# Kernel tuning notes

Hardware: AMD Instinct MI355X
Metric: run time of the kernel (lower is better)

The kernel has to match this reference:

```python
import jax, jax.numpy as jnp
import numpy as np

B, T, NHANDS, DKP = 8, 1024, 2, 128
DM, H, DH, DFF, V, M, L = 1024, 16, 64, 4096, 2000, 256, 2
KEPS = 1e-4  # performer feature-map epsilon


def _orth_proj(key, m, d):
    # Gaussian orthogonal random features (FAVOR+), rows rescaled to chi norms
    n_blocks = int(np.ceil(m / d))
    blocks = []
    for i in range(n_blocks):
        q, _ = jnp.linalg.qr(jax.random.normal(jax.random.fold_in(key, i), (d, d)))
        blocks.append(q.T)
    mat = jnp.concatenate(blocks, 0)[:m]
    mult = jnp.linalg.norm(jax.random.normal(jax.random.fold_in(key, 10 ** 6), (m, d)), axis=1)
    return (mat * mult[:, None]).astype(jnp.float32)


def setup_inputs() -> dict:
    key = jax.random.key(0)
    ks = iter(jax.random.split(key, 64))
    w = lambda shape, s=0.02: (jax.random.normal(next(ks), shape) * s).astype(jnp.float32)
    z = lambda *shape: jnp.zeros(shape, jnp.float32)
    o = lambda *shape: jnp.ones(shape, jnp.float32)
    return {
        'x': jax.random.normal(next(ks), (B, T, NHANDS, DKP), dtype=jnp.float32),
        'Win': w((NHANDS * DKP, DM)), 'b_in': z(DM),
        'pe': jax.random.normal(next(ks), (5000, DM), dtype=jnp.float32),
        'ln1_g': o(L, DM), 'ln1_b': z(L, DM),
        'Wq': w((L, DM, DM)), 'bq': z(L, DM),
        'Wk': w((L, DM, DM)), 'bk': z(L, DM),
        'Wv': w((L, DM, DM)), 'bv': z(L, DM),
        'Wo': w((L, DM, DM)), 'bo': z(L, DM),
        'ln2_g': o(L, DM), 'ln2_b': z(L, DM),
        'W1': w((L, DM, DFF)), 'b1': z(L, DFF),
        'W2': w((L, DFF, DM)), 'b2': z(L, DM),
        'Wc': w((DM, V)), 'bc': z(V),
        'Wconv': w((64, DM, 3)), 'bconv': z(64),
        'Waux': w((64, V + 1)), 'baux': z(V + 1),
        'proj': _orth_proj(next(ks), M, DH),
    }


def _ln(x, g, b):
    mu = jnp.mean(x, -1, keepdims=True)
    var = jnp.mean((x - mu) ** 2, -1, keepdims=True)
    return (x - mu) / jnp.sqrt(var + 1e-5) * g + b


def _feats(data, proj, is_query):
    # FAVOR+ softmax kernel features, data: (B,H,T,DH) -> (B,H,T,M)
    dn = DH ** -0.25
    ratio = M ** -0.5
    dd = jnp.einsum('bhnd,md->bhnm', data, proj) * dn
    diag = jnp.sum(data ** 2, -1, keepdims=True) * 0.5 * dn * dn
    if is_query:
        stab = jnp.max(dd, -1, keepdims=True)
    else:
        stab = jnp.max(dd, (-1, -2), keepdims=True)
    return ratio * (jnp.exp(dd - diag - jax.lax.stop_gradient(stab)) + KEPS)


def reference(x, Win, b_in, pe, ln1_g, ln1_b, Wq, bq, Wk, bk, Wv, bv, Wo, bo,
              ln2_g, ln2_b, W1, b1, W2, b2, Wc, bc, Wconv, bconv, Waux, baux, proj):
    h = x.reshape(B, T, NHANDS * DKP) @ Win + b_in
    h = h + pe[:T][None]

    def layer(h, i):
        y = _ln(h, ln1_g[i], ln1_b[i])
        q = (y @ Wq[i] + bq[i]).reshape(B, T, H, DH).transpose(0, 2, 1, 3)
        k = (y @ Wk[i] + bk[i]).reshape(B, T, H, DH).transpose(0, 2, 1, 3)
        v = (y @ Wv[i] + bv[i]).reshape(B, T, H, DH).transpose(0, 2, 1, 3)
        qp = _feats(q, proj, True)   # (B,H,T,M)
        kp = _feats(k, proj, False)
        dinv = 1.0 / jnp.einsum('bhnm,bhm->bhn', qp, kp.sum(2))
        ctx = jnp.einsum('bhnm,bhnd->bhmd', kp, v)          # (B,H,M,DH)
        o = jnp.einsum('bhnm,bhmd->bhnd', qp, ctx) * dinv[..., None]
        o = o.transpose(0, 2, 1, 3).reshape(B, T, DM) @ Wo[i] + bo[i]
        h = h + o
        y = _ln(h, ln2_g[i], ln2_b[i])
        ff = jax.nn.gelu(y @ W1[i] + b1[i], approximate=False) @ W2[i] + b2[i]
        return h + ff

    h = layer(h, 0)
    xa = h.transpose(0, 2, 1)  # (B, DM, T)
    xa = jax.lax.conv_general_dilated(xa, Wconv, (1,), 'SAME',
                                      dimension_numbers=('NCH', 'OIH', 'NCH'))
    xa = xa + bconv[None, :, None]
    aux = xa.transpose(0, 2, 1) @ Waux + baux  # (B, T, V+1)
    h = layer(h, 1)
    gloss = h @ Wc + bc  # (B, T, V)
    return (gloss, aux)
```

## Files before the change

kernel.cpp:

```cpp
#include <hip/hip_runtime.h>
#include <hip/hip_bf16.h>

typedef __attribute__((ext_vector_type(4))) float f32x4;
typedef __attribute__((ext_vector_type(8))) unsigned short u16x8;
typedef __attribute__((ext_vector_type(4))) unsigned short u16x4;
typedef __bf16 bf16x8 __attribute__((ext_vector_type(8)));

#define DEVFN static __device__ __forceinline__

constexpr int CB = 8, CT = 1024, CDM = 1024, CH = 16, CDH = 64, CDFF = 4096, CV = 2000, CM = 256;
constexpr int CNT = CB * CT;
constexpr int CQKV = 3072;
constexpr float CDN = 0.35355339059327373f;
constexpr float CRATIO = 0.0625f;
constexpr float CKEPS = 1e-4f;

DEVFN unsigned short f2bu(float x) {
  __hip_bfloat16 h = __float2bfloat16(x);
  return __builtin_bit_cast(unsigned short, h);
}
DEVFN float b2f(unsigned short u) {
  __hip_bfloat16 h = __builtin_bit_cast(__hip_bfloat16, u);
  return __bfloat162float(h);
}
DEVFN float wredsum(float s) {
#pragma unroll
  for (int ofs = 32; ofs; ofs >>= 1) s += __shfl_xor(s, ofs, 64);
  return s;
}
DEVFN float wredmax(float s) {
#pragma unroll
  for (int ofs = 32; ofs; ofs >>= 1) s = fmaxf(s, __shfl_xor(s, ofs, 64));
  return s;
}
DEVFN void gl_lds16(const void* g, void* l) {
  __builtin_amdgcn_global_load_lds(
      (const __attribute__((address_space(1))) unsigned int*)g,
      (__attribute__((address_space(3))) unsigned int*)l, 16, 0, 0);
}
DEVFN f32x4 mfma16(u16x8 a, u16x8 b, f32x4 c) {
  return __builtin_amdgcn_mfma_f32_16x16x32_bf16(
      __builtin_bit_cast(bf16x8, a), __builtin_bit_cast(bf16x8, b), c, 0, 0, 0);
}
DEVFN u16x8 lds_rd128(unsigned addr) {
  u16x8 r;
  asm volatile("ds_read_b128 %0, %1" : "=v"(r) : "v"(addr));
  return r;
}
DEVFN unsigned lds_addr(const void* p) {
  return (unsigned)(unsigned long)(const __attribute__((address_space(3))) char*)p;
}

#define EPI_BIAS 1
#define EPI_ACCUM 2
#define EPI_GELU 4
#define EPI_OUTBF 8
#define EPI_PE 32
#define EPI_DUP 64

template <int EPI>
__global__ __launch_bounds__(512, 6) void gemm32_k(
    const unsigned short* __restrict__ A, const unsigned short* __restrict__ Bt,
    const float* __restrict__ bias, void* __restrict__ C, void* __restrict__ aux,
    int Mr, int Nr, int Kr, int lda, int ldb, int ldc) {
  __shared__ unsigned short smA[2][128 * 32];
  __shared__ unsigned short smB[2][128 * 32];

  int tid = threadIdx.x, wv = tid >> 6, ll = tid & 63;
  int wm = wv >> 2, wn = wv & 3;
  int m0 = blockIdx.x * 128, n0 = blockIdx.y * 128;
  int fr = ll & 15, f16 = ll >> 4, fk = f16 * 8;

  const char* Ab = (const char*)A;
  const char* Bb = (const char*)Bt;

  unsigned int offA, offB;
  {
    int L = tid * 16;
    int P = L ^ (((L >> 9) & 1) << 5);
    int r = P >> 6, cb = P & 63;
    long rowA = min(m0 + r, Mr - 1);
    offA = (unsigned)(rowA * lda * 2 + cb);
    long rowB = min(n0 + r, Nr - 1);
    offB = (unsigned)(rowB * ldb * 2 + cb);
  }
  unsigned aAb = lds_addr(&smA[0][0]), aBb = lds_addr(&smB[0][0]);
  unsigned offArd[4], offBrd[2];
#pragma unroll
  for (int i = 0; i < 4; i++) {
    int r = wm * 64 + i * 16 + fr;
    offArd[i] = aAb + (unsigned)(r * 64 + 2 * (fk ^ (((r >> 3) & 1) << 4)));
  }
#pragma unroll
  for (int j = 0; j < 2; j++) {
    int r = wn * 32 + j * 16 + fr;
    offBrd[j] = aBb + (unsigned)(r * 64 + 2 * (fk ^ (((r >> 3) & 1) << 4)));
  }

  f32x4 acc[4][2] = {};
  int NT = Kr / 32;

#define STG32(PB, KBN)                                                       \
  {                                                                          \
    gl_lds16(Ab + offA + (KBN), &smA[PB][tid * 8]);                          \
    gl_lds16(Bb + offB + (KBN), &smB[PB][tid * 8]);                          \
  }
#define TILE32(PB, KBN)                                                      \
  {                                                                          \
    __builtin_amdgcn_s_barrier();              \
    __builtin_amdgcn_sched_barrier(0);                                       \
    STG32((PB) ^ 1, KBN);                                                    \
    asm volatile("s_waitcnt vmcnt(2)" ::: "memory");                         \
    __builtin_amdgcn_sched_barrier(0);                                       \
    __builtin_amdgcn_s_barrier();                 \
    __builtin_amdgcn_sched_barrier(0);                                       \
    u16x8 a[4], b0, b1;                                                      \
    _Pragma("unroll") for (int i = 0; i < 4; i++)                            \
        a[i] = lds_rd128(offArd[i] + (PB)*8192);                             \
    b0 = lds_rd128(offBrd[0] + (PB)*8192);                                   \
    b1 = lds_rd128(offBrd[1] + (PB)*8192);                                   \
    asm volatile("s_waitcnt lgkmcnt(1)" ::: "memory");                       \
    __builtin_amdgcn_sched_barrier(0);                                       \
    __builtin_amdgcn_s_setprio(1);                                           \
    _Pragma("unroll") for (int i = 0; i < 4; i++)                            \
        acc[i][0] = mfma16(a[i], b0, acc[i][0]);                             \
    __builtin_amdgcn_s_setprio(0);                                           \
    asm volatile("s_waitcnt lgkmcnt(0)" ::: "memory");                       \
    __builtin_amdgcn_sched_barrier(0);                                       \
    __builtin_amdgcn_s_setprio(1);                                           \
    _Pragma("unroll") for (int i = 0; i < 4; i++)                            \
        acc[i][1] = mfma16(a[i], b1, acc[i][1]);                             \
    __builtin_amdgcn_s_setprio(0);                                           \
  }

  STG32(0, 0);
  for (int t = 0; t < NT; t += 2) {
    long kb1 = (long)(t + 1) * 64;
    long kb2 = (long)min(t + 2, NT - 1) * 64;
    TILE32(0, kb1);
    TILE32(1, kb2);
  }
  asm volatile("s_waitcnt vmcnt(0)" ::: "memory");
  __builtin_amdgcn_sched_barrier(0);
#undef TILE32
#undef STG32

#pragma unroll
  for (int i = 0; i < 4; i++) {
#pragma unroll
    for (int j = 0; j < 2; j++) {
#pragma unroll
      for (int e = 0; e < 4; e++) {
        int gr = m0 + wm * 64 + i * 16 + f16 * 4 + e;
        int gc = n0 + wn * 32 + j * 16 + fr;
        if (gr < Mr && gc < Nr) {
          float v = acc[i][j][e];
          if (EPI & EPI_BIAS) v += bias[gc];
          if (EPI & EPI_GELU) v = 0.5f * v * (1.0f + erff(v * 0.70710678118f));
          if (EPI & EPI_PE) v += ((const float*)aux)[((long)(gr & 1023) << 10) + gc];
          long idx = (long)gr * ldc + gc;
          if (EPI & EPI_ACCUM) v += ((float*)C)[idx];
          if (EPI & EPI_OUTBF) ((unsigned short*)C)[idx] = f2bu(v);
          else ((float*)C)[idx] = v;
          if (EPI & EPI_DUP) ((unsigned short*)aux)[idx] = f2bu(v);
        }
      }
    }
  }
}

template <int EPI>
__global__ __launch_bounds__(512, 4) void gemm128_k(
    const unsigned short* __restrict__ A, const unsigned short* __restrict__ Bt,
    const float* __restrict__ bias, void* __restrict__ C, void* __restrict__ aux,
    int Mr, int Nr, int Kr, int lda, int ldb, int ldc) {
  __shared__ unsigned short smA[2][128 * 64];
  __shared__ unsigned short smB[2][128 * 64];

  int tid = threadIdx.x, wv = tid >> 6, ll = tid & 63;
  int wm = wv >> 2, wn = wv & 3;
  int m0 = blockIdx.x * 128, n0 = blockIdx.y * 128;
  int fr = ll & 15, f16 = ll >> 4, fk = f16 * 8;

  const char* Ab = (const char*)A;
  const char* Bb = (const char*)Bt;

  unsigned int offA[2], offB[2];
#pragma unroll
  for (int ro = 0; ro < 2; ro++) {
    int L = (ro * 512 + tid) * 16;
    int P = L ^ (((L >> 9) & 1) << 5);
    int kh = P >> 13, rem = P & 8191;
    int r = rem >> 6, cb = rem & 63;
    long rowA = min(m0 + r, Mr - 1);
    offA[ro] = (unsigned)((rowA * lda + kh * 32) * 2 + cb);
    long rowB = min(n0 + r, Nr - 1);
    offB[ro] = (unsigned)((rowB * ldb + kh * 32) * 2 + cb);
  }
  unsigned aAb = lds_addr(&smA[0][0]), aBb = lds_addr(&smB[0][0]);
  unsigned offArd[4], offBrd[2];
#pragma unroll
  for (int i = 0; i < 4; i++) {
    int r = wm * 64 + i * 16 + fr;
    offArd[i] = aAb + (unsigned)(r * 64 + 2 * (fk ^ (((r >> 3) & 1) << 4)));
  }
#pragma unroll
  for (int j = 0; j < 2; j++) {
    int r = wn * 32 + j * 16 + fr;
    offBrd[j] = aBb + (unsigned)(r * 64 + 2 * (fk ^ (((r >> 3) & 1) << 4)));
  }

  f32x4 acc[4][2] = {};
  int NT = Kr / 64;

#define STGALL(PB, KBN)                                                      \
  {                                                                          \
    _Pragma("unroll") for (int ro = 0; ro < 2; ro++)                         \
        gl_lds16(Ab + offA[ro] + (KBN), &smA[PB][(ro * 512 + wv * 64) * 8]); \
    _Pragma("unroll") for (int ro = 0; ro < 2; ro++)                         \
        gl_lds16(Bb + offB[ro] + (KBN), &smB[PB][(ro * 512 + wv * 64) * 8]); \
  }
#define TILE(PB, KBN)                                                        \
  {                                                                          \
    __builtin_amdgcn_s_barrier();                                            \
    __builtin_amdgcn_sched_barrier(0);                                       \
    STGALL((PB) ^ 1, KBN);                                                   \
    asm volatile("s_waitcnt vmcnt(4)" ::: "memory");                         \
    __builtin_amdgcn_sched_barrier(0);                                       \
    __builtin_amdgcn_s_barrier();                                            \
    __builtin_amdgcn_sched_barrier(0);                                       \
    u16x8 a0[4], b0[2], a1[4], b1[2];                                        \
    _Pragma("unroll") for (int i = 0; i < 4; i++)                            \
        a0[i] = lds_rd128(offArd[i] + (PB)*16384);                           \
    _Pragma("unroll") for (int j = 0; j < 2; j++)                            \
        b0[j] = lds_rd128(offBrd[j] + (PB)*16384);                           \
    _Pragma("unroll") for (int i = 0; i < 4; i++)                            \
        a1[i] = lds_rd128(offArd[i] + (PB)*16384 + 8192);                    \
    _Pragma("unroll") for (int j = 0; j < 2; j++)                            \
        b1[j] = lds_rd128(offBrd[j] + (PB)*16384 + 8192);                    \
    asm volatile("s_waitcnt lgkmcnt(6)" ::: "memory");                       \
    __builtin_amdgcn_sched_barrier(0);                                       \
    __builtin_amdgcn_s_setprio(1);                                           \
    _Pragma("unroll") for (int i = 0; i < 4; i++) {                          \
      acc[i][0] = mfma16(a0[i], b0[0], acc[i][0]);                           \
      acc[i][1] = mfma16(a0[i], b0[1], acc[i][1]);                           \
    }                                                                        \
    __builtin_amdgcn_s_setprio(0);                                           \
    asm volatile("s_waitcnt lgkmcnt(0)" ::: "memory");                       \
    __builtin_amdgcn_sched_barrier(0);                                       \
    __builtin_amdgcn_s_setprio(1);                                           \
    _Pragma("unroll") for (int i = 0; i < 4; i++) {                          \
      acc[i][0] = mfma16(a1[i], b1[0], acc[i][0]);                           \
      acc[i][1] = mfma16(a1[i], b1[1], acc[i][1]);                           \
    }                                                                        \
    __builtin_amdgcn_s_setprio(0);                                           \
  }

  STGALL(0, 0);
  for (int t = 0; t < NT; t += 2) {
    long kb1 = (long)(t + 1) * 128;
    long kb2 = (long)min(t + 2, NT - 1) * 128;
    TILE(0, kb1);
    TILE(1, kb2);
  }
  asm volatile("s_waitcnt vmcnt(0)" ::: "memory");
  __builtin_amdgcn_sched_barrier(0);
#undef TILE
#undef STGALL

#pragma unroll
  for (int i = 0; i < 4; i++) {
#pragma unroll
    for (int j = 0; j < 2; j++) {
#pragma unroll
      for (int e = 0; e < 4; e++) {
        int gr = m0 + wm * 64 + i * 16 + f16 * 4 + e;
        int gc = n0 + wn * 32 + j * 16 + fr;
        if (gr < Mr && gc < Nr) {
          float v = acc[i][j][e];
          if (EPI & EPI_BIAS) v += bias[gc];
          if (EPI & EPI_GELU) v = 0.5f * v * (1.0f + erff(v * 0.70710678118f));
          if (EPI & EPI_PE) v += ((const float*)aux)[((long)(gr & 1023) << 10) + gc];
          long idx = (long)gr * ldc + gc;
          if (EPI & EPI_ACCUM) v += ((float*)C)[idx];
          if (EPI & EPI_OUTBF) ((unsigned short*)C)[idx] = f2bu(v);
          else ((float*)C)[idx] = v;
          if (EPI & EPI_DUP) ((unsigned short*)aux)[idx] = f2bu(v);
        }
      }
    }
  }
}

template <int EPI, int MB, int NB>
__global__ __launch_bounds__(256) void gemm_k(
    const unsigned short* __restrict__ Aall, const unsigned short* __restrict__ Btall,
    const float* __restrict__ bias, void* __restrict__ Call,
    int Mr, int Nr, int Kr, int lda, int ldb, int ldc, int bdiv,
    long As1, long As2, long Bs1, long Bs2, long Cs1, long Cs2) {
  __shared__ unsigned short smA[MB * 32];
  __shared__ unsigned short smB[NB * 32];
  constexpr int WRN = (MB == 128 && NB == 128) ? 2 : (MB == 128 ? 4 : 1);
  constexpr int WCN = 4 / WRN;
  constexpr int MT = MB / WRN, NTW = NB / WCN;
  constexpr int AF = MT / 16, BF = NTW / 16;
  int bz = blockIdx.z;
  const unsigned short* A = Aall + (long)(bz / bdiv) * As1 + (long)(bz % bdiv) * As2;
  const unsigned short* Bt = Btall + (long)(bz / bdiv) * Bs1 + (long)(bz % bdiv) * Bs2;
  long coff = (long)(bz / bdiv) * Cs1 + (long)(bz % bdiv) * Cs2;

  int tid = threadIdx.x, wv = tid >> 6, ll = tid & 63;
  int m0 = blockIdx.x * MB, n0 = blockIdx.y * NB;
  int sr = tid >> 2, sc = (tid & 3) * 8;
  long ar0 = min(m0 + sr, Mr - 1);
  long ar1 = (MB == 128) ? min(m0 + sr + 64, (long)Mr - 1) : 0;
  long br0 = min(n0 + sr, Nr - 1);
  long br1 = (NB == 128) ? min(n0 + sr + 64, (long)Nr - 1) : 0;
  unsigned short* lA0 = &smA[(wv * 16) * 32];
  unsigned short* lA1 = &smA[(64 + wv * 16) * 32];
  unsigned short* lB0 = &smB[(wv * 16) * 32];
  unsigned short* lB1 = &smB[(64 + wv * 16) * 32];

  f32x4 acc[AF][BF] = {};
  int wr = (WRN == 1) ? 0 : ((WRN == 2) ? (wv >> 1) * MT : wv * MT);
  int wc = (WCN == 1) ? 0 : ((WCN == 2) ? (wv & 1) * NTW : wv * NTW);
  int fr = ll & 15, fk = (ll >> 4) * 8;

  for (int k0 = 0; k0 < Kr; k0 += 32) {
    __syncthreads();
    gl_lds16(A + ar0 * lda + k0 + sc, lA0);
    if (MB == 128) gl_lds16(A + ar1 * lda + k0 + sc, lA1);
    gl_lds16(Bt + br0 * ldb + k0 + sc, lB0);
    if (NB == 128) gl_lds16(Bt + br1 * ldb + k0 + sc, lB1);
    __syncthreads();
    u16x8 af[AF], bfr[BF];
#pragma unroll
    for (int i = 0; i < AF; i++) af[i] = *(const u16x8*)&smA[(wr + i * 16 + fr) * 32 + fk];
#pragma unroll
    for (int j = 0; j < BF; j++) bfr[j] = *(const u16x8*)&smB[(wc + j * 16 + fr) * 32 + fk];
#pragma unroll
    for (int i = 0; i < AF; i++)
#pragma unroll
      for (int j = 0; j < BF; j++) acc[i][j] = mfma16(af[i], bfr[j], acc[i][j]);
  }

#pragma unroll
  for (int i = 0; i < AF; i++) {
#pragma unroll
    for (int j = 0; j < BF; j++) {
#pragma unroll
      for (int e = 0; e < 4; e++) {
        int gr = m0 + wr + i * 16 + (ll >> 4) * 4 + e;
        int gc = n0 + wc + j * 16 + (ll & 15);
        if (gr < Mr && gc < Nr) {
          float v = acc[i][j][e];
          if (EPI & EPI_BIAS) v += bias[gc];
          long idx = coff + (long)gr * ldc + gc;
          if (EPI & EPI_OUTBF) ((unsigned short*)Call)[idx] = f2bu(v);
          else ((float*)Call)[idx] = v;
        }
      }
    }
  }
}

DEVFN void feat_dd(const unsigned short* __restrict__ src, const unsigned short* __restrict__ projc,
                   unsigned short* ldsq, unsigned short* ldsp, int b, int t0, int hh,
                   f32x4 acc[16]) {
  int tid = threadIdx.x, wv = tid >> 6, ll = tid & 63;
#pragma unroll
  for (int p = 0; p < 2; p++) {
    int r = p * 64 + (tid >> 3), c8 = (tid & 7) * 8;
    *(u16x8*)&ldsq[r * 72 + c8] =
        *(const u16x8*)&src[((long)b * CT + t0 + r) * CQKV + hh * CDH + c8];
  }
#pragma unroll
  for (int p = 0; p < 4; p++) {
    int r = p * 64 + (tid >> 3), c8 = (tid & 7) * 8;
    *(u16x8*)&ldsp[r * 72 + c8] = *(const u16x8*)&projc[r * 64 + c8];
  }
  __syncthreads();
  int fr = ll & 15, fk = (ll >> 4) * 8;
#pragma unroll
  for (int ks = 0; ks < 2; ks++) {
    u16x8 af = *(const u16x8*)&ldsq[(wv * 16 + fr) * 72 + ks * 32 + fk];
#pragma unroll
    for (int j = 0; j < 16; j++) {
      u16x8 bf = *(const u16x8*)&ldsp[(j * 16 + fr) * 72 + ks * 32 + fk];
      acc[j] = mfma16(af, bf, acc[j]);
    }
  }
}

__global__ __launch_bounds__(512, 4) void kstab_f(const unsigned short* __restrict__ kb,
                                                  const unsigned short* __restrict__ projc,
                                                  const unsigned short* __restrict__ vb,
                                                  float* __restrict__ part,
                                                  unsigned short* __restrict__ vt) {
  extern __shared__ char dynsm[];
  unsigned short* ldsq = (unsigned short*)dynsm;
  unsigned short* ldsp = (unsigned short*)(dynsm + 18432);
  __shared__ float smx[8];
  int tid = threadIdx.x;
  int bh = blockIdx.x >> 3, chunk = blockIdx.x & 7;
  int b = bh >> 4, hh = bh & 15;
  int t0 = chunk * 128;
  f32x4 acc[16] = {};
  feat_dd(kb, projc, ldsq, ldsp, b, t0, hh, acc);
  float mx = -3.4e38f;
#pragma unroll
  for (int j = 0; j < 16; j++)
#pragma unroll
    for (int e = 0; e < 4; e++) mx = fmaxf(mx, acc[j][e]);
  mx = wredmax(mx);
  int wv = tid >> 6;
  if ((tid & 63) == 0) smx[wv] = mx;
  __syncthreads();
  if (tid == 0) {
    float m2 = smx[0];
#pragma unroll
    for (int i = 1; i < 8; i++) m2 = fmaxf(m2, smx[i]);
    part[blockIdx.x] = m2;
  }
#pragma unroll
  for (int p = 0; p < 2; p++) {
    int r = p * 64 + (tid >> 3), c8 = (tid & 7) * 8;
    *(u16x8*)&ldsq[r * 72 + c8] =
        *(const u16x8*)&vb[((long)b * CT + t0 + r) * CQKV + hh * CDH + c8];
  }
  __syncthreads();
  int d = tid >> 3, tz = (tid & 7) * 16;
  unsigned short o1[8], o2[8];
#pragma unroll
  for (int e = 0; e < 8; e++) {
    o1[e] = ldsq[(tz + e) * 72 + d];
    o2[e] = ldsq[(tz + 8 + e) * 72 + d];
  }
  long vbase = ((long)bh * CDH + d) * CT + t0 + tz;
  *(u16x8*)&vt[vbase] = *(u16x8*)&o1[0];
  *(u16x8*)&vt[vbase + 8] = *(u16x8*)&o2[0];
}

__global__ __launch_bounds__(512, 4) void featk_f(const unsigned short* __restrict__ kb,
                                                  const unsigned short* __restrict__ projc,
                                                  const float* __restrict__ part,
                                                  unsigned short* __restrict__ kpt,
                                                  float* __restrict__ kspart) {
  extern __shared__ char dynsm[];
  unsigned short* ldsq = (unsigned short*)dynsm;
  unsigned short* ldsp = (unsigned short*)(dynsm + 18432);
  unsigned short* ldso = (unsigned short*)dynsm;
  int tid = threadIdx.x, wv = tid >> 6, ll = tid & 63;
  int bh = blockIdx.x >> 3, chunk = blockIdx.x & 7;
  int b = bh >> 4, hh = bh & 15;
  float st = part[bh * 8];
#pragma unroll
  for (int i = 1; i < 8; i++) st = fmaxf(st, part[bh * 8 + i]);
  f32x4 acc[16] = {};
  feat_dd(kb, projc, ldsq, ldsp, b, chunk * 128, hh, acc);
  int fr = ll & 15, g = ll >> 4;
  float diag[4];
#pragma unroll
  for (int e = 0; e < 4; e++) {
    int row = wv * 16 + g * 4 + e;
    u16x4 kv = *(const u16x4*)&ldsq[row * 72 + fr * 4];
    float s = 0;
#pragma unroll
    for (int z = 0; z < 4; z++) { float f = b2f(kv[z]); s += f * f; }
#pragma unroll
    for (int o = 1; o < 16; o <<= 1) s += __shfl_xor(s, o, 64);
    diag[e] = s * (0.5f * CDN * CDN);
  }
  __syncthreads();
#pragma unroll
  for (int j = 0; j < 16; j++)
#pragma unroll
    for (int e = 0; e < 4; e++) {
      float v = CRATIO * (expf(acc[j][e] - diag[e] - st) + CKEPS);
      ldso[(j * 16 + fr) * 136 + wv * 16 + g * 4 + e] = f2bu(v);
    }
  __syncthreads();
  int m = tid >> 1, seg = (tid & 1) * 64;
  long base = ((long)bh * CM + m) * CT + chunk * 128;
  float ks = 0;
#pragma unroll
  for (int z = 0; z < 8; z++) {
    u16x8 v8 = *(u16x8*)&ldso[m * 136 + seg + z * 8];
    *(u16x8*)&kpt[base + seg + z * 8] = v8;
#pragma unroll
    for (int w = 0; w < 8; w++) ks += b2f(v8[w]);
  }
  ks += __shfl_xor(ks, 1, 64);
  if ((tid & 1) == 0) kspart[((long)bh * 8 + chunk) * CM + m] = ks;
}

__global__ __launch_bounds__(512, 4) void featqo_f(const unsigned short* __restrict__ qb,
                                                   const unsigned short* __restrict__ projc,
                                                   const float* __restrict__ kspart,
                                                   const unsigned short* __restrict__ ctxall,
                                                   unsigned short* __restrict__ obuf) {
  extern __shared__ char dynsm[];
  unsigned short* ldsq = (unsigned short*)dynsm;
  unsigned short* ldsp = (unsigned short*)(dynsm + 18432);
  unsigned short* ldso = (unsigned short*)dynsm;
  float* ldks = (float*)(dynsm + 67584);
  float* ldinv = (float*)(dynsm + 68608);
  int tid = threadIdx.x, wv = tid >> 6, ll = tid & 63;
  int bh = blockIdx.x >> 3, chunk = blockIdx.x & 7;
  int b = bh >> 4, hh = bh & 15;
  int t0 = chunk * 128;
  if (tid < 256) {
    float s = 0;
#pragma unroll
    for (int c = 0; c < 8; c++) s += kspart[((long)bh * 8 + c) * CM + tid];
    ldks[tid] = s;
  }
  f32x4 acc[16] = {};
  feat_dd(qb, projc, ldsq, ldsp, b, t0, hh, acc);
  int fr = ll & 15, g = ll >> 4, fk = g * 8;
  float rmax[4], diag[4];
#pragma unroll
  for (int e = 0; e < 4; e++) {
    float mx = acc[0][e];
#pragma unroll
    for (int j = 1; j < 16; j++) mx = fmaxf(mx, acc[j][e]);
#pragma unroll
    for (int o = 1; o < 16; o <<= 1) mx = fmaxf(mx, __shfl_xor(mx, o, 64));
    rmax[e] = mx;
    int row = wv * 16 + g * 4 + e;
    u16x4 qv = *(const u16x4*)&ldsq[row * 72 + fr * 4];
    float s = 0;
#pragma unroll
    for (int z = 0; z < 4; z++) { float f = b2f(qv[z]); s += f * f; }
#pragma unroll
    for (int o = 1; o < 16; o <<= 1) s += __shfl_xor(s, o, 64);
    diag[e] = s * (0.5f * CDN * CDN);
  }
  __syncthreads();
#pragma unroll
  for (int j = 0; j < 16; j++)
#pragma unroll
    for (int e = 0; e < 4; e++) {
      float v = CRATIO * (expf(acc[j][e] - diag[e] - rmax[e]) + CKEPS);
      ldso[(wv * 16 + g * 4 + e) * 264 + j * 16 + fr] = f2bu(v);
    }
  __syncthreads();
  {
    int row = tid >> 2, seg = (tid & 3) * 64;
    float dot = 0;
#pragma unroll
    for (int z = 0; z < 8; z++) {
      u16x8 v8 = *(u16x8*)&ldso[row * 264 + seg + z * 8];
#pragma unroll
      for (int w = 0; w < 8; w++) dot += b2f(v8[w]) * ldks[seg + z * 8 + w];
    }
    dot += __shfl_xor(dot, 1, 64);
    dot += __shfl_xor(dot, 2, 64);
    if ((tid & 3) == 0) ldinv[row] = 1.0f / dot;
  }
  const unsigned short* ctxb = ctxall + (long)bh * 16384;
  f32x4 ao[4] = {};
#pragma unroll
  for (int ks = 0; ks < 8; ks++) {
    u16x8 af = *(const u16x8*)&ldso[(wv * 16 + fr) * 264 + ks * 32 + fk];
#pragma unroll
    for (int j = 0; j < 4; j++) {
      u16x8 bf = *(const u16x8*)&ctxb[(j * 16 + fr) * 256 + ks * 32 + fk];
      ao[j] = mfma16(af, bf, ao[j]);
    }
  }
  __syncthreads();
#pragma unroll
  for (int j = 0; j < 4; j++)
#pragma unroll
    for (int e = 0; e < 4; e++) {
      int r = wv * 16 + g * 4 + e;
      float v = ao[j][e] * ldinv[r];
      obuf[((long)b * CT + t0 + r) * CDM + hh * CDH + j * 16 + fr] = f2bu(v);
    }
}

__global__ __launch_bounds__(256) void ln_k(const float* __restrict__ h,
                                            const float* __restrict__ g,
                                            const float* __restrict__ b,
                                            unsigned short* __restrict__ y) {
  int wv = threadIdx.x >> 6, ll = threadIdx.x & 63;
  long row = (long)blockIdx.x * 4 + wv;
  const float* hr = h + row * CDM;
  f32x4 x[4];
#pragma unroll
  for (int i = 0; i < 4; i++) x[i] = *(const f32x4*)&hr[ll * 16 + i * 4];
  float s = 0;
#pragma unroll
  for (int i = 0; i < 4; i++)
#pragma unroll
    for (int e = 0; e < 4; e++) s += x[i][e];
  float mu = wredsum(s) * (1.f / CDM);
  float v = 0;
#pragma unroll
  for (int i = 0; i < 4; i++)
#pragma unroll
    for (int e = 0; e < 4; e++) {
      float d = x[i][e] - mu;
      v += d * d;
    }
  float inv = rsqrtf(wredsum(v) * (1.f / CDM) + 1e-5f);
  unsigned short o[16];
#pragma unroll
  for (int i = 0; i < 4; i++)
#pragma unroll
    for (int e = 0; e < 4; e++) {
      int c = ll * 16 + i * 4 + e;
      o[i * 4 + e] = f2bu((x[i][e] - mu) * inv * g[c] + b[c]);
    }
  *(u16x8*)&y[row * CDM + ll * 16] = *(u16x8*)&o[0];
  *(u16x8*)&y[row * CDM + ll * 16 + 8] = *(u16x8*)&o[8];
}

__global__ __launch_bounds__(256) void f2b_k(const float* __restrict__ in,
                                             unsigned short* __restrict__ out, long n) {
  long i = ((long)blockIdx.x * 256 + threadIdx.x) * 4;
  if (i >= n) return;
  f32x4 v = *(const f32x4*)&in[i];
  unsigned short o[4];
#pragma unroll
  for (int e = 0; e < 4; e++) o[e] = f2bu(v[e]);
  *(u16x4*)&out[i] = *(u16x4*)&o[0];
}

__global__ __launch_bounds__(256) void tconvz_k(const float* __restrict__ in,
                                                unsigned short* __restrict__ out, int R, int C,
                                                long szs, long dzs) {
  const float* src = in + (long)blockIdx.z * szs;
  unsigned short* dst = out + (long)blockIdx.z * dzs;
  __shared__ float tile[32][33];
  int r0 = blockIdx.x * 32, c0 = blockIdx.y * 32;
  int tr = threadIdx.x >> 5, tc = threadIdx.x & 31;
#pragma unroll
  for (int p = 0; p < 4; p++) {
    int r = r0 + p * 8 + tr, c = c0 + tc;
    tile[p * 8 + tr][tc] = (r < R && c < C) ? src[(long)r * C + c] : 0.f;
  }
  __syncthreads();
#pragma unroll
  for (int p = 0; p < 4; p++) {
    int c = c0 + p * 8 + tr, r = r0 + tc;
    if (c < C && r < R) dst[(long)c * R + r] = f2bu(tile[tc][p * 8 + tr]);
  }
}

__global__ __launch_bounds__(256) void tconv4_k(const float* __restrict__ Wq,
                                                const float* __restrict__ Wk,
                                                const float* __restrict__ Wv,
                                                const float* __restrict__ Wo,
                                                unsigned short* __restrict__ out) {
  int w = blockIdx.z & 3, l = blockIdx.z >> 2;
  const float* src = (w == 0 ? Wq : w == 1 ? Wk : w == 2 ? Wv : Wo) + (long)l * 1048576;
  unsigned short* dst = out + ((long)l * 4 + w) * 1048576;
  __shared__ float tile[32][33];
  int r0 = blockIdx.x * 32, c0 = blockIdx.y * 32;
  int tr = threadIdx.x >> 5, tc = threadIdx.x & 31;
#pragma unroll
  for (int p = 0; p < 4; p++) {
    int r = r0 + p * 8 + tr, c = c0 + tc;
    tile[p * 8 + tr][tc] = src[(long)r * 1024 + c];
  }
  __syncthreads();
#pragma unroll
  for (int p = 0; p < 4; p++) {
    int c = c0 + p * 8 + tr, r = r0 + tc;
    dst[(long)c * 1024 + r] = f2bu(tile[tc][p * 8 + tr]);
  }
}

__global__ __launch_bounds__(256) void wconv_k(const float* __restrict__ W,
                                               unsigned short* __restrict__ out) {
  int idx = blockIdx.x * 256 + threadIdx.x;
  int r = idx >> 16, rem = idx & 65535, oc = rem >> 10, ic = rem & 1023;
  out[idx] = f2bu(W[oc * 3072 + ic * 3 + r]);
}

__global__ __launch_bounds__(256) void convmix_k(const float* __restrict__ Y,
                                                 const float* __restrict__ bc,
                                                 unsigned short* __restrict__ xab) {
  long t = (long)blockIdx.x * 4 + (threadIdx.x >> 6);
  int oc = threadIdx.x & 63;
  int tb = (int)(t & 1023);
  float v = Y[t * 192 + 64 + oc] + bc[oc];
  if (tb != 0) v += Y[(t - 1) * 192 + oc];
  if (tb != 1023) v += Y[(t + 1) * 192 + 128 + oc];
  xab[t * 64 + oc] = f2bu(v);
}

__global__ __launch_bounds__(256) void projc_k(const float* __restrict__ p,
                                               unsigned short* __restrict__ out) {
  int i = blockIdx.x * 256 + threadIdx.x;
  out[i] = f2bu(p[i] * CDN);
}

__global__ __launch_bounds__(256) void catb_k(const float* __restrict__ q,
                                              const float* __restrict__ k,
                                              const float* __restrict__ v,
                                              float* __restrict__ o) {
  int l = blockIdx.y;
  int i = blockIdx.x * 256 + threadIdx.x;
  float val = i < 1024 ? q[l * CDM + i] : (i < 2048 ? k[l * CDM + i - 1024] : v[l * CDM + i - 2048]);
  o[l * CQKV + i] = val;
}

#define LAUNCH_GEMM(EPI, MB, NB, A, Bt, bias, C, Mr, Nr, Kr, lda, ldb, ldc, nb, bdiv, As1, As2, Bs1, Bs2, Cs1, Cs2) \
  gemm_k<EPI, MB, NB><<<dim3(((Mr) + (MB)-1) / (MB), ((Nr) + (NB)-1) / (NB), (nb)), 256, 0, stream>>>( \
      (const unsigned short*)(A), (const unsigned short*)(Bt), (bias), (void*)(C),               \
      (Mr), (Nr), (Kr), (lda), (ldb), (ldc), (bdiv), (long)(As1), (long)(As2), (long)(Bs1),      \
      (long)(Bs2), (long)(Cs1), (long)(Cs2))

#define LAUNCH_G1(EPI, A, Bt, bias, C, AUX, Mr, Nr, Kr, lda, ldb, ldc)                           \
  gemm128_k<EPI><<<dim3(((Mr) + 127) / 128, ((Nr) + 127) / 128), 512, 0, stream>>>(              \
      (const unsigned short*)(A), (const unsigned short*)(Bt), (bias), (void*)(C), (void*)(AUX), \
      (Mr), (Nr), (Kr), (lda), (ldb), (ldc))

#define LAUNCH_G32(EPI, A, Bt, bias, C, AUX, Mr, Nr, Kr, lda, ldb, ldc)                          \
  gemm32_k<EPI><<<dim3(((Mr) + 127) / 128, ((Nr) + 127) / 128), 512, 0, stream>>>(               \
      (const unsigned short*)(A), (const unsigned short*)(Bt), (bias), (void*)(C), (void*)(AUX), \
      (Mr), (Nr), (Kr), (lda), (ldb), (ldc))

extern "C" void kernel_launch(void* const* d_in, const int* in_sizes, int n_in,
                              void* d_out, int out_size, void* d_ws, size_t ws_size,
                              hipStream_t stream) {
  const float* x = (const float*)d_in[0];
  const float* Win = (const float*)d_in[1];
  const float* b_in = (const float*)d_in[2];
  const float* pe = (const float*)d_in[3];
  const float* ln1_g = (const float*)d_in[4];
  const float* ln1_b = (const float*)d_in[5];
  const float* Wq = (const float*)d_in[6];
  const float* bq = (const float*)d_in[7];
  const float* Wk = (const float*)d_in[8];
  const float* bk = (const float*)d_in[9];
  const float* Wv = (const float*)d_in[10];
  const float* bv = (const float*)d_in[11];
  const float* Wo = (const float*)d_in[12];
  const float* bo = (const float*)d_in[13];
  const float* ln2_g = (const float*)d_in[14];
  const float* ln2_b = (const float*)d_in[15];
  const float* W1 = (const float*)d_in[16];
  const float* b1 = (const float*)d_in[17];
  const float* W2 = (const float*)d_in[18];
  const float* b2 = (const float*)d_in[19];
  const float* Wc = (const float*)d_in[20];
  const float* bc = (const float*)d_in[21];
  const float* Wconv = (const float*)d_in[22];
  const float* bconv = (const float*)d_in[23];
  const float* Waux = (const float*)d_in[24];
  const float* baux = (const float*)d_in[25];
  const float* proj = (const float*)d_in[26];
  float* out = (float*)d_out;

  char* wsp = (char*)d_ws;
  size_t off = 0;
  auto take = [&](size_t bytes) {
    char* p = wsp + off;
    off = (off + bytes + 255) & ~(size_t)255;
    return p;
  };
  float* h_f = (float*)take(33554432);
  unsigned short* y_bf = (unsigned short*)take(16777216);
  unsigned short* qkv_bf = (unsigned short*)take(50331648);
  unsigned short* kpt_bf = (unsigned short*)take(67108864);
  unsigned short* ff_bf = (unsigned short*)take(67108864);
  unsigned short* ctx_bf = (unsigned short*)take(4194304);
  float* kspart_f = (float*)take(1048576);
  float* kstab_f_buf = (float*)take(4096);
  float* ycv_f = (float*)take(6291456);
  unsigned short* xabf = (unsigned short*)take(1048576);
  float* bqkv_f = (float*)take(24576);
  unsigned short* hbf = (unsigned short*)take(16777216);
  unsigned short* xbf = (unsigned short*)take(4194304);
  unsigned short* win_t = (unsigned short*)take(524288);
  unsigned short* wqkvo_t = (unsigned short*)take(16777216);
  unsigned short* w1_t = (unsigned short*)take(16777216);
  unsigned short* w2_t = (unsigned short*)take(16777216);
  unsigned short* wc_t = (unsigned short*)take(4096000);
  unsigned short* projc = (unsigned short*)take(32768);
  unsigned short* wconv_t = (unsigned short*)take(393216);
  unsigned short* waux_t = (unsigned short*)take(256128);
  unsigned short* vt_bf = y_bf;
  unsigned short* o_bf = y_bf;
  (void)in_sizes; (void)n_in; (void)out_size; (void)ws_size;

  f2b_k<<<2048, 256, 0, stream>>>(x, xbf, (long)CNT * 256);
  tconvz_k<<<dim3(8, 32, 1), 256, 0, stream>>>(Win, win_t, 256, 1024, 0, 0);
  tconv4_k<<<dim3(32, 32, 8), 256, 0, stream>>>(Wq, Wk, Wv, Wo, wqkvo_t);
  tconvz_k<<<dim3(32, 128, 2), 256, 0, stream>>>(W1, w1_t, 1024, 4096, 4194304, 4194304);
  tconvz_k<<<dim3(128, 32, 2), 256, 0, stream>>>(W2, w2_t, 4096, 1024, 4194304, 4194304);
  tconvz_k<<<dim3(32, 63, 1), 256, 0, stream>>>(Wc, wc_t, 1024, 2000, 0, 0);
  tconvz_k<<<dim3(2, 63, 1), 256, 0, stream>>>(Waux, waux_t, 64, 2001, 0, 0);
  catb_k<<<dim3(12, 2), 256, 0, stream>>>(bq, bk, bv, bqkv_f);
  wconv_k<<<768, 256, 0, stream>>>(Wconv, wconv_t);
  projc_k<<<64, 256, 0, stream>>>(proj, projc);

  LAUNCH_G1(EPI_BIAS | EPI_PE, xbf, win_t, b_in, h_f, pe, CNT, CDM, 256, 256, 256, CDM);

  for (int l = 0; l < 2; l++) {
    const unsigned short* wqkv_t = wqkvo_t + (long)(l * 4) * 1048576;
    const unsigned short* wo_t = wqkvo_t + (long)(l * 4 + 3) * 1048576;

    ln_k<<<2048, 256, 0, stream>>>(h_f, ln1_g + l * CDM, ln1_b + l * CDM, y_bf);
    LAUNCH_G32(EPI_BIAS | EPI_OUTBF, y_bf, wqkv_t, bqkv_f + l * CQKV, qkv_bf, nullptr, CNT, CQKV, CDM, CDM, CDM, CQKV);

    kstab_f<<<1024, 512, 55296, stream>>>(qkv_bf + 1024, projc, qkv_bf + 2048, kstab_f_buf, vt_bf);
    featk_f<<<1024, 512, 69632, stream>>>(qkv_bf + 1024, projc, kstab_f_buf, kpt_bf, kspart_f);
    LAUNCH_GEMM(EPI_OUTBF, 64, 128, vt_bf, kpt_bf, nullptr, ctx_bf, CDH, CM, CT, CT, CT, CM, 128, CH,
                (long)CH * CDH * CT, (long)CDH * CT, (long)CH * CM * CT, (long)CM * CT,
                (long)CH * CDH * CM, (long)CDH * CM);
    featqo_f<<<1024, 512, 69120, stream>>>(qkv_bf, projc, kspart_f, ctx_bf, o_bf);
    LAUNCH_G1(EPI_BIAS | EPI_ACCUM, o_bf, wo_t, bo + l * CDM, h_f, nullptr, CNT, CDM, CDM, CDM, CDM, CDM);

    ln_k<<<2048, 256, 0, stream>>>(h_f, ln2_g + l * CDM, ln2_b + l * CDM, y_bf);
    LAUNCH_G32(EPI_BIAS | EPI_GELU | EPI_OUTBF, y_bf, w1_t + (long)l * 4194304, b1 + l * CDFF, ff_bf, nullptr,
               CNT, CDFF, CDM, CDM, CDM, CDFF);
    LAUNCH_G1(EPI_BIAS | EPI_ACCUM | EPI_DUP, ff_bf, w2_t + (long)l * 4194304, b2 + l * CDM, h_f, hbf,
              CNT, CDM, CDFF, CDFF, CDFF, CDM);

    if (l == 0) {
      LAUNCH_GEMM(0, 128, 128, hbf, wconv_t, nullptr, ycv_f, CNT, 192, CDM, CDM, CDM, 192, 1, 1, 0, 0, 0, 0, 0, 0);
      convmix_k<<<2048, 256, 0, stream>>>(ycv_f, bconv, xabf);
      LAUNCH_GEMM(EPI_BIAS, 128, 128, xabf, waux_t, baux, out + 16384000, CNT, CV + 1, 64, 64, 64, CV + 1, 1, 1, 0, 0, 0, 0, 0, 0);
    }
  }

  LAUNCH_G1(EPI_BIAS, hbf, wc_t, bc, out, nullptr, CNT, CV, CDM, CDM, CDM, CV);
}
```

Measured before the change: 1.140 ms.

## Load GEMM B fragments directly from global into registers, bypassing LDS

The 128x128 K=32 GEMM used for the QKV and FFN1 projections no longer stages the weight (B) tile through shared memory. Each wave now loads its own B MFMA fragments straight from global memory with dwordx4 loads, while the A tile is still double-buffered in LDS. The goal is to halve LDS traffic and footprint and to drop the B LDS reads. In exchange, each B row is fetched by all waves sharing it, so global and L2 traffic rises, and the B load is issued only one stage ahead, with vmcnt waits that must be ordered correctly.

```diff
diff --git a/kernel.cpp b/kernel.cpp
--- a/kernel.cpp
+++ b/kernel.cpp
@@ -47,6 +47,11 @@
   asm volatile("ds_read_b128 %0, %1" : "=v"(r) : "v"(addr));
   return r;
 }
+DEVFN u16x8 gld128(const void* p) {
+  u16x8 r;
+  asm volatile("global_load_dwordx4 %0, %1, off" : "=v"(r) : "v"(p));
+  return r;
+}
 DEVFN unsigned lds_addr(const void* p) {
   return (unsigned)(unsigned long)(const __attribute__((address_space(3))) char*)p;
 }
@@ -59,12 +64,11 @@
 #define EPI_DUP 64
 
 template <int EPI>
-__global__ __launch_bounds__(512, 6) void gemm32_k(
+__global__ __launch_bounds__(512, 6) void gemm32b_k(
     const unsigned short* __restrict__ A, const unsigned short* __restrict__ Bt,
     const float* __restrict__ bias, void* __restrict__ C, void* __restrict__ aux,
     int Mr, int Nr, int Kr, int lda, int ldb, int ldc) {
   __shared__ unsigned short smA[2][128 * 32];
-  __shared__ unsigned short smB[2][128 * 32];
 
   int tid = threadIdx.x, wv = tid >> 6, ll = tid & 63;
   int wm = wv >> 2, wn = wv & 3;
@@ -74,58 +78,54 @@
   const char* Ab = (const char*)A;
   const char* Bb = (const char*)Bt;
 
-  unsigned int offA, offB;
+  unsigned int offA;
   {
     int L = tid * 16;
     int P = L ^ (((L >> 9) & 1) << 5);
     int r = P >> 6, cb = P & 63;
     long rowA = min(m0 + r, Mr - 1);
     offA = (unsigned)(rowA * lda * 2 + cb);
-    long rowB = min(n0 + r, Nr - 1);
-    offB = (unsigned)(rowB * ldb * 2 + cb);
-  }
-  unsigned aAb = lds_addr(&smA[0][0]), aBb = lds_addr(&smB[0][0]);
-  unsigned offArd[4], offBrd[2];
+  }
+  unsigned aAb = lds_addr(&smA[0][0]);
+  unsigned offArd[4];
 #pragma unroll
   for (int i = 0; i < 4; i++) {
     int r = wm * 64 + i * 16 + fr;
     offArd[i] = aAb + (unsigned)(r * 64 + 2 * (fk ^ (((r >> 3) & 1) << 4)));
   }
+  long bOff[2];
 #pragma unroll
   for (int j = 0; j < 2; j++) {
-    int r = wn * 32 + j * 16 + fr;
-    offBrd[j] = aBb + (unsigned)(r * 64 + 2 * (fk ^ (((r >> 3) & 1) << 4)));
+    long row = min(n0 + wn * 32 + j * 16 + fr, Nr - 1);
+    bOff[j] = (row * (long)ldb + fk) * 2;
   }
 
   f32x4 acc[4][2] = {};
   int NT = Kr / 32;
 
-#define STG32(PB, KBN)                                                       \
-  {                                                                          \
-    gl_lds16(Ab + offA + (KBN), &smA[PB][tid * 8]);                          \
-    gl_lds16(Bb + offB + (KBN), &smB[PB][tid * 8]);                          \
-  }
-#define TILE32(PB, KBN)                                                      \
+#define TILE32B(PB, KBN, KBC)                                                \
   {                                                                          \
     __builtin_amdgcn_s_barrier();              \
     __builtin_amdgcn_sched_barrier(0);                                       \
-    STG32((PB) ^ 1, KBN);                                                    \
-    asm volatile("s_waitcnt vmcnt(2)" ::: "memory");                         \
+    u16x8 b0 = gld128(Bb + bOff[0] + (KBC));                                 \
+    u16x8 b1 = gld128(Bb + bOff[1] + (KBC));                                 \
+    gl_lds16(Ab + offA + (KBN), &smA[(PB) ^ 1][tid * 8]);                    \
+    asm volatile("s_waitcnt vmcnt(3)" ::: "memory");        \
     __builtin_amdgcn_sched_barrier(0);                                       \
     __builtin_amdgcn_s_barrier();                 \
     __builtin_amdgcn_sched_barrier(0);                                       \
-    u16x8 a[4], b0, b1;                                                      \
+    u16x8 a[4];                                                              \
     _Pragma("unroll") for (int i = 0; i < 4; i++)                            \
         a[i] = lds_rd128(offArd[i] + (PB)*8192);                             \
-    b0 = lds_rd128(offBrd[0] + (PB)*8192);                                   \
-    b1 = lds_rd128(offBrd[1] + (PB)*8192);                                   \
-    asm volatile("s_waitcnt lgkmcnt(1)" ::: "memory");                       \
+    asm volatile("s_waitcnt lgkmcnt(0)" ::: "memory");                       \
+    __builtin_amdgcn_sched_barrier(0);                                       \
+    asm volatile("s_waitcnt vmcnt(2)" ::: "memory");          \
     __builtin_amdgcn_sched_barrier(0);                                       \
     __builtin_amdgcn_s_setprio(1);                                           \
     _Pragma("unroll") for (int i = 0; i < 4; i++)                            \
         acc[i][0] = mfma16(a[i], b0, acc[i][0]);                             \
     __builtin_amdgcn_s_setprio(0);                                           \
-    asm volatile("s_waitcnt lgkmcnt(0)" ::: "memory");                       \
+    asm volatile("s_waitcnt vmcnt(1)" ::: "memory");          \
     __builtin_amdgcn_sched_barrier(0);                                       \
     __builtin_amdgcn_s_setprio(1);                                           \
     _Pragma("unroll") for (int i = 0; i < 4; i++)                            \
@@ -133,17 +133,17 @@
     __builtin_amdgcn_s_setprio(0);                                           \
   }
 
-  STG32(0, 0);
+  gl_lds16(Ab + offA, &smA[0][tid * 8]);
   for (int t = 0; t < NT; t += 2) {
-    long kb1 = (long)(t + 1) * 64;
+    long kc1 = (long)t * 64, kc2 = (long)(t + 1) * 64;
+    long kb1 = kc2;
     long kb2 = (long)min(t + 2, NT - 1) * 64;
-    TILE32(0, kb1);
-    TILE32(1, kb2);
+    TILE32B(0, kb1, kc1);
+    TILE32B(1, kb2, kc2);
   }
   asm volatile("s_waitcnt vmcnt(0)" ::: "memory");
   __builtin_amdgcn_sched_barrier(0);
-#undef TILE32
-#undef STG32
+#undef TILE32B
 
 #pragma unroll
   for (int i = 0; i < 4; i++) {
@@ -719,8 +719,8 @@
       (const unsigned short*)(A), (const unsigned short*)(Bt), (bias), (void*)(C), (void*)(AUX), \
       (Mr), (Nr), (Kr), (lda), (ldb), (ldc))
 
-#define LAUNCH_G32(EPI, A, Bt, bias, C, AUX, Mr, Nr, Kr, lda, ldb, ldc)                          \
-  gemm32_k<EPI><<<dim3(((Mr) + 127) / 128, ((Nr) + 127) / 128), 512, 0, stream>>>(               \
+#define LAUNCH_G32B(EPI, A, Bt, bias, C, AUX, Mr, Nr, Kr, lda, ldb, ldc)                         \
+  gemm32b_k<EPI><<<dim3(((Mr) + 127) / 128, ((Nr) + 127) / 128), 512, 0, stream>>>(              \
       (const unsigned short*)(A), (const unsigned short*)(Bt), (bias), (void*)(C), (void*)(AUX), \
       (Mr), (Nr), (Kr), (lda), (ldb), (ldc))
 
@@ -806,7 +806,7 @@
     const unsigned short* wo_t = wqkvo_t + (long)(l * 4 + 3) * 1048576;
 
     ln_k<<<2048, 256, 0, stream>>>(h_f, ln1_g + l * CDM, ln1_b + l * CDM, y_bf);
-    LAUNCH_G32(EPI_BIAS | EPI_OUTBF, y_bf, wqkv_t, bqkv_f + l * CQKV, qkv_bf, nullptr, CNT, CQKV, CDM, CDM, CDM, CQKV);
+    LAUNCH_G32B(EPI_BIAS | EPI_OUTBF, y_bf, wqkv_t, bqkv_f + l * CQKV, qkv_bf, nullptr, CNT, CQKV, CDM, CDM, CDM, CQKV);
 
     kstab_f<<<1024, 512, 55296, stream>>>(qkv_bf + 1024, projc, qkv_bf + 2048, kstab_f_buf, vt_bf);
     featk_f<<<1024, 512, 69632, stream>>>(qkv_bf + 1024, projc, kstab_f_buf, kpt_bf, kspart_f);
@@ -817,8 +817,8 @@
     LAUNCH_G1(EPI_BIAS | EPI_ACCUM, o_bf, wo_t, bo + l * CDM, h_f, nullptr, CNT, CDM, CDM, CDM, CDM, CDM);
 
     ln_k<<<2048, 256, 0, stream>>>(h_f, ln2_g + l * CDM, ln2_b + l * CDM, y_bf);
-    LAUNCH_G32(EPI_BIAS | EPI_GELU | EPI_OUTBF, y_bf, w1_t + (long)l * 4194304, b1 + l * CDFF, ff_bf, nullptr,
-               CNT, CDFF, CDM, CDM, CDM, CDFF);
+    LAUNCH_G32B(EPI_BIAS | EPI_GELU | EPI_OUTBF, y_bf, w1_t + (long)l * 4194304, b1 + l * CDFF, ff_bf, nullptr,
+                CNT, CDFF, CDM, CDM, CDM, CDFF);
     LAUNCH_G1(EPI_BIAS | EPI_ACCUM | EPI_DUP, ff_bf, w2_t + (long)l * 4194304, b2 + l * CDM, h_f, hbf,
               CNT, CDM, CDFF, CDFF, CDFF, CDM);
 
```

Measured after the change: 1.338 ms. +17.3%, slower.
